# Kernel tuning notes

Measured on AMD Instinct MI355X. Metric: run time of the kernel, lower is better.

## Reference

```python
import jax, jax.numpy as jnp
import numpy as np

B, S, D_MODEL, H = 2, 2048, 512, 8
DH = D_MODEL // H  # dim per head
NEG_INF = 1e9


def setup_inputs() -> dict:
    key = jax.random.key(0)
    ks = jax.random.split(key, 8)
    sc = 0.05
    return {
        "query": jax.random.normal(ks[0], (B, S, D_MODEL), jnp.float32),
        "key": jax.random.normal(ks[1], (B, S, D_MODEL), jnp.float32),
        "value": jax.random.normal(ks[2], (B, S, D_MODEL), jnp.float32),
        "mask": jnp.zeros((B, 1, S, S), jnp.float32),
        "wq": jax.random.normal(ks[3], (D_MODEL, D_MODEL), jnp.float32) * sc,
        "bq": jnp.zeros((D_MODEL,), jnp.float32),
        "wk": jax.random.normal(ks[4], (D_MODEL, D_MODEL), jnp.float32) * sc,
        "bk": jnp.zeros((D_MODEL,), jnp.float32),
        "wv": jax.random.normal(ks[5], (D_MODEL, D_MODEL), jnp.float32) * sc,
        "bv": jnp.zeros((D_MODEL,), jnp.float32),
        "wo": jax.random.normal(ks[6], (D_MODEL, D_MODEL), jnp.float32) * sc,
        "bo": jnp.zeros((D_MODEL,), jnp.float32),
    }


def _split_heads(x):
    # (B, S, D_MODEL) -> (B, H, S, DH)
    b, s, _ = x.shape
    return x.reshape(b, s, H, DH).transpose(0, 2, 1, 3)


def reference(query, key, value, mask, wq, bq, wk, bk, wv, bv, wo, bo):
    q = _split_heads(query @ wq + bq)
    k = _split_heads(key @ wk + bk)
    v = _split_heads(value @ wv + bv)
    # scaled dot-product attention; full (B, H, S, S) scores as in original
    scores = jnp.einsum("bhqd,bhkd->bhqk", q, k) / jnp.sqrt(jnp.float32(DH))
    scores = scores + mask * (-NEG_INF)
    weights = jax.nn.softmax(scores, axis=-1)  # dropout inactive (rate=0 / eval)
    attn = jnp.einsum("bhqk,bhkd->bhqd", weights, v)
    # merge heads: (B, H, S, DH) -> (B, S, D_MODEL)
    b = attn.shape[0]
    merged = attn.transpose(0, 2, 1, 3).reshape(b, -1, D_MODEL)
    return merged @ wo + bo
```

## Files before the change

kernel.cpp:

```cpp
#include <hip/hip_runtime.h>
#include <hip/hip_bf16.h>

typedef unsigned short u16;
typedef unsigned int u32;
typedef __bf16 bf16x8 __attribute__((ext_vector_type(8)));
typedef float f32x4 __attribute__((ext_vector_type(4)));
typedef u16 u16x8 __attribute__((ext_vector_type(8)));
typedef u32 u32x2 __attribute__((ext_vector_type(2)));

#define S_LEN 2048
#define DMODEL 512
#define NHEAD 8
#define DHEAD 64
#define KSPLIT 2
#define KRANGE (S_LEN / KSPLIT)
#define QSCALE 0.1803368801111204f
#define MASKC 1.4426950409e9f
#define RESCALE_THR 8.0f

static __device__ __forceinline__ u16 f2bf(float f) {
    union { float f; unsigned u; } cv; cv.f = f;
    unsigned u = cv.u;
    return (u16)((u + 0x7fffu + ((u >> 16) & 1u)) >> 16);
}
static __device__ __forceinline__ u32 pk2bf(float a, float b) {
    union { __hip_bfloat162 h; u32 u; } cv;
    float2 f2; f2.x = a; f2.y = b;
    cv.h = __float22bfloat162_rn(f2);
    return cv.u;
}
static __device__ __forceinline__ bf16x8 ld8(const u16* p) {
    return *(const bf16x8*)p;
}
static __device__ __forceinline__ float fmax3(float a, float b, float c) {
    return __builtin_fmaxf(__builtin_fmaxf(a, b), c);
}

__global__ __launch_bounds__(256) void prep_kernel(
    const float* __restrict__ q, const float* __restrict__ k, const float* __restrict__ v,
    const float* __restrict__ w0, const float* __restrict__ w1,
    const float* __restrict__ w2, const float* __restrict__ w3,
    const float* __restrict__ mask,
    u16* __restrict__ Aqkv, u16* __restrict__ wtall, int* __restrict__ flags) {
    const int p = blockIdx.x;
    const int tid = threadIdx.x;
    __shared__ float t[32][33];
    __shared__ int wred[4];
    if (p < 3072) {
        const int z = p >> 10, px = p & 1023;
        const float* in = (z == 0) ? q : (z == 1) ? k : v;
        u16* o = Aqkv + (long)z * 2097152;
        long i = ((long)px * 256 + tid) * 8;
        f32x4 a = *(const f32x4*)(in + i);
        f32x4 b = *(const f32x4*)(in + i + 4);
        u16x8 r;
#pragma unroll
        for (int j = 0; j < 4; ++j) { r[j] = f2bf(a[j]); r[4 + j] = f2bf(b[j]); }
        *(u16x8*)(o + i) = r;
    } else if (p < 4096) {
        const int p2 = p - 3072;
        const int z = p2 >> 8, rem = p2 & 255, by = rem >> 4, bx = rem & 15;
        const float* in = (z == 0) ? w0 : (z == 1) ? w1 : (z == 2) ? w2 : w3;
        u16* o = wtall + (long)(((z + 1) & 3)) * 262144;
        const int tx = tid & 31, ty = tid >> 5;
#pragma unroll
        for (int i = 0; i < 4; ++i)
            t[ty + 8 * i][tx] = in[(by * 32 + ty + 8 * i) * DMODEL + bx * 32 + tx];
        __syncthreads();
#pragma unroll
        for (int i = 0; i < 4; ++i)
            o[(bx * 32 + ty + 8 * i) * DMODEL + by * 32 + tx] = f2bf(t[tx][ty + 8 * i]);
    } else {
        const int bid = p - 4096;
        const int b = bid >> 10, qt = (bid >> 5) & 31, kt = bid & 31;
        const int r = tid >> 2, cs = tid & 3;
        const float* mp = mask + ((long)(b * S_LEN + qt * 64 + r)) * S_LEN + kt * 64 + cs * 16;
        int nz = 0;
#pragma unroll
        for (int j = 0; j < 4; ++j) {
            f32x4 a = *(const f32x4*)(mp + j * 4);
            nz |= (a[0] != 0.f) | (a[1] != 0.f) | (a[2] != 0.f) | (a[3] != 0.f);
        }
        unsigned long long ball = __ballot(nz);
        if ((tid & 63) == 0) wred[tid >> 6] = (ball != 0ull) ? 1 : 0;
        __syncthreads();
        if (tid == 0) flags[bid] = wred[0] | wred[1] | wred[2] | wred[3];
    }
}

template <bool F32OUT, int TM>
static __device__ __forceinline__ void gemm_body(const u16* __restrict__ A,
                                                 const u16* __restrict__ Wt,
                                                 const float* __restrict__ bias,
                                                 void* __restrict__ Cp, float oscale,
                                                 bool vtout) {
    const int lane = threadIdx.x & 63;
    const int wave = threadIdx.x >> 6;
    const int wr = wave >> 1, wc = wave & 1;
    const int m0 = blockIdx.y * (TM * 32) + wr * (TM * 16);
    const int n0 = blockIdx.x * 64 + wc * 32;
    const int cidx = lane & 15;
    const int kg = lane >> 4;

    const u16* aptr[TM];
    const u16* bptr[2];
#pragma unroll
    for (int t = 0; t < TM; ++t)
        aptr[t] = A + (long)(m0 + t * 16 + cidx) * DMODEL + kg * 8;
#pragma unroll
    for (int t = 0; t < 2; ++t)
        bptr[t] = Wt + (long)(n0 + t * 16 + cidx) * DMODEL + kg * 8;

    const f32x4 fz = {0.f, 0.f, 0.f, 0.f};
    f32x4 acc[TM][2];
#pragma unroll
    for (int i = 0; i < TM; ++i)
#pragma unroll
        for (int j = 0; j < 2; ++j) acc[i][j] = fz;

#pragma unroll 4
    for (int k0 = 0; k0 < 512; k0 += 32) {
        bf16x8 a[TM], b[2];
#pragma unroll
        for (int t = 0; t < TM; ++t) a[t] = ld8(aptr[t] + k0);
#pragma unroll
        for (int t = 0; t < 2; ++t) b[t] = ld8(bptr[t] + k0);
#pragma unroll
        for (int i = 0; i < TM; ++i)
#pragma unroll
            for (int j = 0; j < 2; ++j)
                acc[i][j] = __builtin_amdgcn_mfma_f32_16x16x32_bf16(a[i], b[j], acc[i][j], 0, 0, 0);
    }

    if (vtout) {
        const int bb = m0 >> 11;
#pragma unroll
        for (int j = 0; j < 2; ++j) {
            int col = n0 + j * 16 + cidx;
            float bv = bias[col];
            u16* vt = (u16*)Cp + (((long)(bb * 8 + (col >> 6))) * 64 + (col & 63)) * S_LEN;
#pragma unroll
            for (int i = 0; i < TM; ++i) {
                int s = (m0 + i * 16 + kg * 4) & (S_LEN - 1);
                u32x2 d;
                d[0] = pk2bf(acc[i][j][0] + bv, acc[i][j][1] + bv);
                d[1] = pk2bf(acc[i][j][2] + bv, acc[i][j][3] + bv);
                *(u32x2*)(vt + s) = d;
            }
        }
        return;
    }

#pragma unroll
    for (int j = 0; j < 2; ++j) {
        int col = n0 + j * 16 + cidx;
        float bv = bias[col];
#pragma unroll
        for (int i = 0; i < TM; ++i) {
#pragma unroll
            for (int r = 0; r < 4; ++r) {
                int row = m0 + i * 16 + kg * 4 + r;
                float val = (acc[i][j][r] + bv) * oscale;
                if (F32OUT) {
                    ((float*)Cp)[(long)row * DMODEL + col] = val;
                } else {
                    ((u16*)Cp)[(long)row * DMODEL + col] = f2bf(val);
                }
            }
        }
    }
}

__global__ __launch_bounds__(256) void qkv_gemm_kernel(
    const u16* __restrict__ Aqkv,
    const u16* __restrict__ wtall,
    const float* __restrict__ bq, const float* __restrict__ bk, const float* __restrict__ bv,
    u16* __restrict__ Q, u16* __restrict__ K, u16* __restrict__ Vt) {
    const u16* A = Aqkv + (long)blockIdx.z * 2097152;
    const u16* W = wtall + (long)(blockIdx.z + 1) * 262144;
    const float* b;
    u16* C;
    float sc = 1.f;
    bool vt = false;
    if (blockIdx.z == 0) { b = bq; C = Q; sc = QSCALE; }
    else if (blockIdx.z == 1) { b = bk; C = K; }
    else { b = bv; C = Vt; vt = true; }
    gemm_body<false, 4>(A, W, b, C, sc, vt);
}

__global__ __launch_bounds__(256) void out_gemm_kernel(const u16* __restrict__ A,
                                                       const u16* __restrict__ Wt,
                                                       const float* __restrict__ bias,
                                                       float* __restrict__ C) {
    gemm_body<true, 2>(A, Wt, bias, C, 1.f, false);
}

__global__ __launch_bounds__(256) void attn_kernel(const u16* __restrict__ Q,
                                                   const u16* __restrict__ K,
                                                   const u16* __restrict__ Vt,
                                                   const float* __restrict__ mask,
                                                   const int* __restrict__ flags,
                                                   u16* __restrict__ Opart,
                                                   float* __restrict__ ML) {
    const int tid = threadIdx.x;
    const int lane = tid & 63;
    const int wave = tid >> 6;
    const int cidx = lane & 15;
    const int kg = lane >> 4;
    const int bh = blockIdx.y;
    const int b = bh >> 3, h = bh & 7;
    const int q0 = blockIdx.x * 64 + wave * 16;
    const int z = blockIdx.z;
    const int k0z = z * KRANGE;

    __shared__ u16 kt_lds[2][64 * 64];
    __shared__ u16 vt_lds[2][64 * 64];
    __shared__ u16 p_lds[4][16 * 64];
    u16* pw = p_lds[wave];

    const long qbase = ((long)(b * S_LEN + q0 + cidx)) * DMODEL + h * DHEAD + kg * 8;
    bf16x8 aq0 = ld8(Q + qbase);
    bf16x8 aq1 = ld8(Q + qbase + 32);

    bf16x8 onesf;
    {
        u16x8 t8;
        u16 ob = (cidx == 0) ? (u16)0x3F80 : (u16)0;
#pragma unroll
        for (int j = 0; j < 8; ++j) t8[j] = ob;
        onesf = *(bf16x8*)&t8;
    }

    const f32x4 fz = {0.f, 0.f, 0.f, 0.f};
    f32x4 acc[4];
#pragma unroll
    for (int nt = 0; nt < 4; ++nt) acc[nt] = fz;
    f32x4 accL = fz;
    float mrow = -1e30f;

    const int krow0 = tid >> 3, kseg0 = tid & 7;
    const int krow1 = krow0 + 32;
    const u16* kgbase = K + ((long)(b * S_LEN + k0z)) * DMODEL + h * DHEAD;
    const u16* vgbase = Vt + ((long)bh * DHEAD) * S_LEN + k0z;
    const int kd0 = krow0 * 64 + (((kseg0 ^ (krow0 & 7))) << 3);
    const int kd1 = krow1 * 64 + (((kseg0 ^ (krow1 & 7))) << 3);
    const int* flagrow = flags + b * 1024 + blockIdx.x * 32 + z * (KRANGE / 64);
    const int NIT = KRANGE / 64;

    const u16* kp0 = kgbase + (long)krow0 * DMODEL + kseg0 * 8;
    const u16* kp1 = kgbase + (long)krow1 * DMODEL + kseg0 * 8;
    const u16* vp0 = vgbase + (long)krow0 * S_LEN + kseg0 * 8;
    const u16* vp1 = vgbase + (long)krow1 * S_LEN + kseg0 * 8;

    u16x8 rk0 = *(const u16x8*)kp0;
    u16x8 rk1 = *(const u16x8*)kp1;
    u16x8 rv0 = *(const u16x8*)vp0;
    u16x8 rv1 = *(const u16x8*)vp1;
    *(u16x8*)&kt_lds[0][kd0] = rk0;
    *(u16x8*)&kt_lds[0][kd1] = rk1;
    *(u16x8*)&vt_lds[0][kd0] = rv0;
    *(u16x8*)&vt_lds[0][kd1] = rv1;
    rk0 = *(const u16x8*)(kp0 + 64 * DMODEL);
    rk1 = *(const u16x8*)(kp1 + 64 * DMODEL);
    rv0 = *(const u16x8*)(vp0 + 64);
    rv1 = *(const u16x8*)(vp1 + 64);
    __syncthreads();

    for (int it = 0; it < NIT; ++it) {
        const int cur = it & 1;
        if (it + 1 < NIT) {
            u16* kn = kt_lds[cur ^ 1];
            u16* vn = vt_lds[cur ^ 1];
            *(u16x8*)&kn[kd0] = rk0;
            *(u16x8*)&kn[kd1] = rk1;
            *(u16x8*)&vn[kd0] = rv0;
            *(u16x8*)&vn[kd1] = rv1;
            if (it + 2 < NIT) {
                const int t2 = (it + 2) * 64;
                rk0 = *(const u16x8*)(kp0 + (long)t2 * DMODEL);
                rk1 = *(const u16x8*)(kp1 + (long)t2 * DMODEL);
                rv0 = *(const u16x8*)(vp0 + t2);
                rv1 = *(const u16x8*)(vp1 + t2);
            }
        }
        const int flg = flagrow[it];
        const u16* kb = kt_lds[cur];
        const u16* vb = vt_lds[cur];

        f32x4 sacc[4];
#pragma unroll
        for (int ct = 0; ct < 4; ++ct) sacc[ct] = fz;
        __builtin_amdgcn_s_setprio(1);
#pragma unroll
        for (int ct = 0; ct < 4; ++ct) {
            int r = ct * 16 + cidx;
            bf16x8 kv0 = ld8(&kb[r * 64 + ((kg ^ (r & 7)) << 3)]);
            bf16x8 kv1 = ld8(&kb[r * 64 + (((4 ^ kg) ^ (r & 7)) << 3)]);
            sacc[ct] = __builtin_amdgcn_mfma_f32_16x16x32_bf16(kv0, aq0, sacc[ct], 0, 0, 0);
            sacc[ct] = __builtin_amdgcn_mfma_f32_16x16x32_bf16(kv1, aq1, sacc[ct], 0, 0, 0);
        }
        __builtin_amdgcn_s_setprio(0);
        if (flg) {
            const float* mb = mask + ((long)(b * S_LEN + q0 + cidx)) * S_LEN + k0z + it * 64 + kg * 4;
#pragma unroll
            for (int ct = 0; ct < 4; ++ct) {
                f32x4 mv = *(const f32x4*)(mb + ct * 16);
#pragma unroll
                for (int r = 0; r < 4; ++r) sacc[ct][r] -= MASKC * mv[r];
            }
        }
        float t0 = fmax3(sacc[0][0], sacc[0][1], sacc[0][2]);
        float t1 = fmax3(sacc[0][3], sacc[1][0], sacc[1][1]);
        float t2 = fmax3(sacc[1][2], sacc[1][3], sacc[2][0]);
        float t3 = fmax3(sacc[2][1], sacc[2][2], sacc[2][3]);
        float t4 = fmax3(sacc[3][0], sacc[3][1], sacc[3][2]);
        float mx = __builtin_fmaxf(fmax3(fmax3(t0, t1, t2), t3, t4), sacc[3][3]);
        mx = fmaxf(mx, __shfl_xor(mx, 16));
        mx = fmaxf(mx, __shfl_xor(mx, 32));
        if (mx > mrow + RESCALE_THR) {
            float mnew = fmaxf(mrow, mx);
            float alpha = __builtin_amdgcn_exp2f(mrow - mnew);
            mrow = mnew;
            accL = accL * alpha;
#pragma unroll
            for (int nt = 0; nt < 4; ++nt) acc[nt] = acc[nt] * alpha;
        }
#pragma unroll
        for (int ct = 0; ct < 4; ++ct)
#pragma unroll
            for (int r = 0; r < 4; ++r)
                sacc[ct][r] = __builtin_amdgcn_exp2f(sacc[ct][r] - mrow);
#pragma unroll
        for (int ct = 0; ct < 4; ++ct) {
            u32x2 d;
            d[0] = pk2bf(sacc[ct][0], sacc[ct][1]);
            d[1] = pk2bf(sacc[ct][2], sacc[ct][3]);
            int blk = 2 * ct + (kg >> 1);
            *(u32x2*)&pw[cidx * 64 + ((blk ^ (cidx & 7)) << 3) + (kg & 1) * 4] = d;
        }
        bf16x8 pf0 = ld8(&pw[cidx * 64 + ((kg ^ (cidx & 7)) << 3)]);
        bf16x8 pf1 = ld8(&pw[cidx * 64 + (((4 ^ kg) ^ (cidx & 7)) << 3)]);
        __builtin_amdgcn_s_setprio(1);
#pragma unroll
        for (int nt = 0; nt < 4; ++nt) {
            int rr = nt * 16 + cidx;
            bf16x8 v0 = ld8(&vb[rr * 64 + ((kg ^ (rr & 7)) << 3)]);
            bf16x8 v1 = ld8(&vb[rr * 64 + (((4 ^ kg) ^ (rr & 7)) << 3)]);
            acc[nt] = __builtin_amdgcn_mfma_f32_16x16x32_bf16(v0, pf0, acc[nt], 0, 0, 0);
            acc[nt] = __builtin_amdgcn_mfma_f32_16x16x32_bf16(v1, pf1, acc[nt], 0, 0, 0);
        }
        accL = __builtin_amdgcn_mfma_f32_16x16x32_bf16(onesf, pf0, accL, 0, 0, 0);
        accL = __builtin_amdgcn_mfma_f32_16x16x32_bf16(onesf, pf1, accL, 0, 0, 0);
        __builtin_amdgcn_s_setprio(0);
        __syncthreads();
    }
    const long obase = (((long)(z * 16 + bh)) * S_LEN + q0 + cidx) * DHEAD;
#pragma unroll
    for (int nt = 0; nt < 4; ++nt) {
        u32x2 d;
        d[0] = pk2bf(acc[nt][0], acc[nt][1]);
        d[1] = pk2bf(acc[nt][2], acc[nt][3]);
        *(u32x2*)(Opart + obase + nt * 16 + kg * 4) = d;
    }
    if (lane < 16) {
        long mi = ((long)(z * 16 + bh)) * S_LEN + q0 + cidx;
        ML[mi * 2] = mrow;
        ML[mi * 2 + 1] = accL[0];
    }
}

__global__ __launch_bounds__(256) void attn_combine_kernel(const u16* __restrict__ Opart,
                                                           const float* __restrict__ ML,
                                                           u16* __restrict__ Ab) {
    const int tid = threadIdx.x;
    const long rr = (long)blockIdx.x * 32 + (tid >> 3);
    const int c8 = (tid & 7) * 8;
    const int bh = (int)(rr >> 11);
    const int q = (int)(rr & 2047);
    const int b = bh >> 3, h = bh & 7;

    float m[KSPLIT], l[KSPLIT];
#pragma unroll
    for (int zz = 0; zz < KSPLIT; ++zz) {
        long mi = ((long)(zz * 16 + bh)) * S_LEN + q;
        m[zz] = ML[mi * 2];
        l[zz] = ML[mi * 2 + 1];
    }
    float M = m[0];
#pragma unroll
    for (int zz = 1; zz < KSPLIT; ++zz) M = fmaxf(M, m[zz]);
    float L = 0.f, e[KSPLIT];
#pragma unroll
    for (int zz = 0; zz < KSPLIT; ++zz) { e[zz] = exp2f(m[zz] - M); L += e[zz] * l[zz]; }
    float o[8] = {0, 0, 0, 0, 0, 0, 0, 0};
#pragma unroll
    for (int zz = 0; zz < KSPLIT; ++zz) {
        bf16x8 ov = ld8(Opart + (((long)(zz * 16 + bh)) * S_LEN + q) * DHEAD + c8);
#pragma unroll
        for (int j = 0; j < 8; ++j) o[j] += e[zz] * (float)ov[j];
    }
    float invL = 1.f / L;
    u16x8 w;
#pragma unroll
    for (int j = 0; j < 8; ++j) w[j] = f2bf(o[j] * invL);
    *(u16x8*)(Ab + ((long)(b * S_LEN + q)) * DMODEL + h * DHEAD + c8) = w;
}

extern "C" void kernel_launch(void* const* d_in, const int* in_sizes, int n_in,
                              void* d_out, int out_size, void* d_ws, size_t ws_size,
                              hipStream_t stream) {
    const float* q_in = (const float*)d_in[0];
    const float* k_in = (const float*)d_in[1];
    const float* v_in = (const float*)d_in[2];
    const float* mask = (const float*)d_in[3];
    const float* wq = (const float*)d_in[4];
    const float* bq = (const float*)d_in[5];
    const float* wk = (const float*)d_in[6];
    const float* bk = (const float*)d_in[7];
    const float* wv = (const float*)d_in[8];
    const float* bv = (const float*)d_in[9];
    const float* wo = (const float*)d_in[10];
    const float* bo = (const float*)d_in[11];

    u16* ws = (u16*)d_ws;
    u16* Qb = ws;
    u16* Kb = Qb + 2097152;
    u16* Vt = Kb + 2097152;
    u16* wtall = Vt + 2097152;
    u16* Sreg = wtall + 4 * 262144;
    u16* Ab = Sreg + 3 * 2097152;
    int* mflags = (int*)(Ab + 2097152);
    u16* Opart = Sreg;
    float* ML = (float*)(wtall + 262144);

    prep_kernel<<<6144, 256, 0, stream>>>(q_in, k_in, v_in, wq, wk, wv, wo, mask,
                                          Sreg, wtall, mflags);
    qkv_gemm_kernel<<<dim3(8, 32, 3), 256, 0, stream>>>(Sreg, wtall, bq, bk, bv, Qb, Kb, Vt);
    attn_kernel<<<dim3(32, 16, KSPLIT), 256, 0, stream>>>(Qb, Kb, Vt, mask, mflags, Opart, ML);
    attn_combine_kernel<<<1024, 256, 0, stream>>>(Opart, ML, Ab);
    out_gemm_kernel<<<dim3(8, 64), 256, 0, stream>>>(Ab, wtall, bo, (float*)d_out);
}
```

Baseline: 209.1 us.

## Drop split-K attention and combine kernel; add XCD-aware block swizzle to GEMMs

Attention now walks the full key range in one block per query tile and normalizes its output in place, so the partial-output buffer and the separate combine kernel go away. The two GEMM kernels remap block indices so that consecutive row tiles land on the same XCD, which should improve L2 reuse. The online-softmax rescale check now tests the per-lane max with a wave-wide any before doing the cross-lane reduction. The trade-off is that the attention grid shrinks to 512 blocks with twice the serial work each, which may leave the GPU under-occupied.

```diff
diff --git a/kernel.cpp b/kernel.cpp
--- a/kernel.cpp
+++ b/kernel.cpp
@@ -12,8 +12,6 @@
 #define DMODEL 512
 #define NHEAD 8
 #define DHEAD 64
-#define KSPLIT 2
-#define KRANGE (S_LEN / KSPLIT)
 #define QSCALE 0.1803368801111204f
 #define MASKC 1.4426950409e9f
 #define RESCALE_THR 8.0f
@@ -93,12 +91,12 @@
                                                  const u16* __restrict__ Wt,
                                                  const float* __restrict__ bias,
                                                  void* __restrict__ Cp, float oscale,
-                                                 bool vtout) {
+                                                 bool vtout, int bx, int by) {
     const int lane = threadIdx.x & 63;
     const int wave = threadIdx.x >> 6;
     const int wr = wave >> 1, wc = wave & 1;
-    const int m0 = blockIdx.y * (TM * 32) + wr * (TM * 16);
-    const int n0 = blockIdx.x * 64 + wc * 32;
+    const int m0 = by * (TM * 32) + wr * (TM * 16);
+    const int n0 = bx * 64 + wc * 32;
     const int cidx = lane & 15;
     const int kg = lane >> 4;
 
@@ -169,6 +167,14 @@
             }
         }
     }
+}
+
+static __device__ __forceinline__ void xcd_swizzle(int gridX, int gridY, int& bx, int& by) {
+    const int flat = blockIdx.x + gridX * blockIdx.y;
+    const int xcd = flat & 7;
+    const int j = flat >> 3;
+    by = xcd * (gridY >> 3) + j / gridX;
+    bx = j % gridX;
 }
 
 __global__ __launch_bounds__(256) void qkv_gemm_kernel(
@@ -185,14 +191,18 @@
     if (blockIdx.z == 0) { b = bq; C = Q; sc = QSCALE; }
     else if (blockIdx.z == 1) { b = bk; C = K; }
     else { b = bv; C = Vt; vt = true; }
-    gemm_body<false, 4>(A, W, b, C, sc, vt);
+    int bx, by;
+    xcd_swizzle(8, 32, bx, by);
+    gemm_body<false, 4>(A, W, b, C, sc, vt, bx, by);
 }
 
 __global__ __launch_bounds__(256) void out_gemm_kernel(const u16* __restrict__ A,
                                                        const u16* __restrict__ Wt,
                                                        const float* __restrict__ bias,
                                                        float* __restrict__ C) {
-    gemm_body<true, 2>(A, Wt, bias, C, 1.f, false);
+    int bx, by;
+    xcd_swizzle(8, 64, bx, by);
+    gemm_body<true, 2>(A, Wt, bias, C, 1.f, false, bx, by);
 }
 
 __global__ __launch_bounds__(256) void attn_kernel(const u16* __restrict__ Q,
@@ -200,8 +210,7 @@
                                                    const u16* __restrict__ Vt,
                                                    const float* __restrict__ mask,
                                                    const int* __restrict__ flags,
-                                                   u16* __restrict__ Opart,
-                                                   float* __restrict__ ML) {
+                                                   u16* __restrict__ Ab) {
     const int tid = threadIdx.x;
     const int lane = tid & 63;
     const int wave = tid >> 6;
@@ -210,8 +219,6 @@
     const int bh = blockIdx.y;
     const int b = bh >> 3, h = bh & 7;
     const int q0 = blockIdx.x * 64 + wave * 16;
-    const int z = blockIdx.z;
-    const int k0z = z * KRANGE;
 
     __shared__ u16 kt_lds[2][64 * 64];
     __shared__ u16 vt_lds[2][64 * 64];
@@ -240,12 +247,12 @@
 
     const int krow0 = tid >> 3, kseg0 = tid & 7;
     const int krow1 = krow0 + 32;
-    const u16* kgbase = K + ((long)(b * S_LEN + k0z)) * DMODEL + h * DHEAD;
-    const u16* vgbase = Vt + ((long)bh * DHEAD) * S_LEN + k0z;
+    const u16* kgbase = K + ((long)(b * S_LEN)) * DMODEL + h * DHEAD;
+    const u16* vgbase = Vt + ((long)bh * DHEAD) * S_LEN;
     const int kd0 = krow0 * 64 + (((kseg0 ^ (krow0 & 7))) << 3);
     const int kd1 = krow1 * 64 + (((kseg0 ^ (krow1 & 7))) << 3);
-    const int* flagrow = flags + b * 1024 + blockIdx.x * 32 + z * (KRANGE / 64);
-    const int NIT = KRANGE / 64;
+    const int* flagrow = flags + b * 1024 + blockIdx.x * 32;
+    const int NIT = S_LEN / 64;
 
     const u16* kp0 = kgbase + (long)krow0 * DMODEL + kseg0 * 8;
     const u16* kp1 = kgbase + (long)krow1 * DMODEL + kseg0 * 8;
@@ -301,7 +308,7 @@
         }
         __builtin_amdgcn_s_setprio(0);
         if (flg) {
-            const float* mb = mask + ((long)(b * S_LEN + q0 + cidx)) * S_LEN + k0z + it * 64 + kg * 4;
+            const float* mb = mask + ((long)(b * S_LEN + q0 + cidx)) * S_LEN + it * 64 + kg * 4;
 #pragma unroll
             for (int ct = 0; ct < 4; ++ct) {
                 f32x4 mv = *(const f32x4*)(mb + ct * 16);
@@ -314,10 +321,10 @@
         float t2 = fmax3(sacc[1][2], sacc[1][3], sacc[2][0]);
         float t3 = fmax3(sacc[2][1], sacc[2][2], sacc[2][3]);
         float t4 = fmax3(sacc[3][0], sacc[3][1], sacc[3][2]);
-        float mx = __builtin_fmaxf(fmax3(fmax3(t0, t1, t2), t3, t4), sacc[3][3]);
-        mx = fmaxf(mx, __shfl_xor(mx, 16));
-        mx = fmaxf(mx, __shfl_xor(mx, 32));
-        if (mx > mrow + RESCALE_THR) {
+        float mxl = __builtin_fmaxf(fmax3(fmax3(t0, t1, t2), t3, t4), sacc[3][3]);
+        if (__any(mxl > mrow + RESCALE_THR)) {
+            float mx = fmaxf(mxl, __shfl_xor(mxl, 16));
+            mx = fmaxf(mx, __shfl_xor(mx, 32));
             float mnew = fmaxf(mrow, mx);
             float alpha = __builtin_amdgcn_exp2f(mrow - mnew);
             mrow = mnew;
@@ -354,56 +361,16 @@
         __builtin_amdgcn_s_setprio(0);
         __syncthreads();
     }
-    const long obase = (((long)(z * 16 + bh)) * S_LEN + q0 + cidx) * DHEAD;
+    float Lb = __shfl(accL[0], cidx);
+    float invL = 1.f / Lb;
+    const long abase = ((long)(b * S_LEN + q0 + cidx)) * DMODEL + h * DHEAD;
 #pragma unroll
     for (int nt = 0; nt < 4; ++nt) {
         u32x2 d;
-        d[0] = pk2bf(acc[nt][0], acc[nt][1]);
-        d[1] = pk2bf(acc[nt][2], acc[nt][3]);
-        *(u32x2*)(Opart + obase + nt * 16 + kg * 4) = d;
-    }
-    if (lane < 16) {
-        long mi = ((long)(z * 16 + bh)) * S_LEN + q0 + cidx;
-        ML[mi * 2] = mrow;
-        ML[mi * 2 + 1] = accL[0];
-    }
-}
-
-__global__ __launch_bounds__(256) void attn_combine_kernel(const u16* __restrict__ Opart,
-                                                           const float* __restrict__ ML,
-                                                           u16* __restrict__ Ab) {
-    const int tid = threadIdx.x;
-    const long rr = (long)blockIdx.x * 32 + (tid >> 3);
-    const int c8 = (tid & 7) * 8;
-    const int bh = (int)(rr >> 11);
-    const int q = (int)(rr & 2047);
-    const int b = bh >> 3, h = bh & 7;
-
-    float m[KSPLIT], l[KSPLIT];
-#pragma unroll
-    for (int zz = 0; zz < KSPLIT; ++zz) {
-        long mi = ((long)(zz * 16 + bh)) * S_LEN + q;
-        m[zz] = ML[mi * 2];
-        l[zz] = ML[mi * 2 + 1];
-    }
-    float M = m[0];
-#pragma unroll
-    for (int zz = 1; zz < KSPLIT; ++zz) M = fmaxf(M, m[zz]);
-    float L = 0.f, e[KSPLIT];
-#pragma unroll
-    for (int zz = 0; zz < KSPLIT; ++zz) { e[zz] = exp2f(m[zz] - M); L += e[zz] * l[zz]; }
-    float o[8] = {0, 0, 0, 0, 0, 0, 0, 0};
-#pragma unroll
-    for (int zz = 0; zz < KSPLIT; ++zz) {
-        bf16x8 ov = ld8(Opart + (((long)(zz * 16 + bh)) * S_LEN + q) * DHEAD + c8);
-#pragma unroll
-        for (int j = 0; j < 8; ++j) o[j] += e[zz] * (float)ov[j];
-    }
-    float invL = 1.f / L;
-    u16x8 w;
-#pragma unroll
-    for (int j = 0; j < 8; ++j) w[j] = f2bf(o[j] * invL);
-    *(u16x8*)(Ab + ((long)(b * S_LEN + q)) * DMODEL + h * DHEAD + c8) = w;
+        d[0] = pk2bf(acc[nt][0] * invL, acc[nt][1] * invL);
+        d[1] = pk2bf(acc[nt][2] * invL, acc[nt][3] * invL);
+        *(u32x2*)(Ab + abase + nt * 16 + kg * 4) = d;
+    }
 }
 
 extern "C" void kernel_launch(void* const* d_in, const int* in_sizes, int n_in,
@@ -430,13 +397,10 @@
     u16* Sreg = wtall + 4 * 262144;
     u16* Ab = Sreg + 3 * 2097152;
     int* mflags = (int*)(Ab + 2097152);
-    u16* Opart = Sreg;
-    float* ML = (float*)(wtall + 262144);
 
     prep_kernel<<<6144, 256, 0, stream>>>(q_in, k_in, v_in, wq, wk, wv, wo, mask,
                                           Sreg, wtall, mflags);
     qkv_gemm_kernel<<<dim3(8, 32, 3), 256, 0, stream>>>(Sreg, wtall, bq, bk, bv, Qb, Kb, Vt);
-    attn_kernel<<<dim3(32, 16, KSPLIT), 256, 0, stream>>>(Qb, Kb, Vt, mask, mflags, Opart, ML);
-    attn_combine_kernel<<<1024, 256, 0, stream>>>(Opart, ML, Ab);
+    attn_kernel<<<dim3(32, 16), 256, 0, stream>>>(Qb, Kb, Vt, mask, mflags, Ab);
     out_gemm_kernel<<<dim3(8, 64), 256, 0, stream>>>(Ab, wtall, bo, (float*)d_out);
 }
```

Measured after the change: 202.2 us. 3.3% less time.
